# Kernel tuning notes

Hardware: AMD Instinct MI355X
Metric: run time of the kernel (lower is better)

Reference implementation:

```python
import jax, jax.numpy as jnp
import numpy as np

H = 256
W = 256
RADIUS = 1.5
TAU = 1.0
EPS = 1e-8


def _ndc_grid(h, w):
    ys, xs = jnp.meshgrid(jnp.arange(h, dtype=jnp.float32), jnp.arange(w, dtype=jnp.float32), indexing='ij')
    xs = xs / (w - 1) * 2.0 - 1.0
    ys = ys / (h - 1) * 2.0 - 1.0
    return jnp.stack([xs.ravel(), ys.ravel()], 0)  # [2, N]


def _make_rt(key, b, v):
    # near-identity extrinsics: identity rotation + small random translation
    t = jax.random.normal(key, (b, v, 3), dtype=jnp.float32) * 0.05
    rt = jnp.tile(jnp.eye(4, dtype=jnp.float32), (b, v, 1, 1))
    rt = rt.at[:, :, :3, 3].set(t)
    return rt


def setup_inputs() -> dict:
    key = jax.random.key(0)
    ks = jax.random.split(key, 4)
    B, V, C = 2, 3, 32
    depths = jax.random.uniform(ks[0], (B, V, 1, H, W), jnp.float32, 1.0, 3.0)
    feats = jax.random.normal(ks[1], (B, V, C, H, W), jnp.float32)
    K = jnp.tile(jnp.eye(4, dtype=jnp.float32), (B, 1, 1))
    K = K.at[:, 0, 0].set(1.2).at[:, 1, 1].set(1.2)  # NDC-space focal lengths
    src_RTs = _make_rt(ks[2], B, V)
    src_RTinvs = jnp.linalg.inv(src_RTs)
    dst_RTs = _make_rt(ks[3], B, 1)
    dst_RTinvs = jnp.linalg.inv(dst_RTs)
    return {"depths": depths, "feats": feats, "K": K, "src_RTs": src_RTs,
            "src_RTinvs": src_RTinvs, "dst_RTs": dst_RTs, "dst_RTinvs": dst_RTinvs}


def _view_to_world(depth, K_inv, RTinv):
    # depth: [BV, 1, N] -> world homogeneous coords [BV, 4, N]
    grid = _ndc_grid(H, W)                                      # [2, N]
    xy = grid[None] * depth                                     # [BV, 2, N]
    pc = jnp.concatenate([xy, depth, jnp.ones_like(depth)], 1)  # [BV, 4, N]
    cam = jnp.einsum('bij,bjn->bin', K_inv, pc)
    return jnp.einsum('bij,bjn->bin', RTinv, cam)


def _world_to_view(wrld, K, RT):
    cam = jnp.einsum('bij,bjn->bin', RT, wrld)
    proj = jnp.einsum('bij,bjn->bin', K, cam)
    z = proj[:, 2:3]
    xy = proj[:, 0:2] / (z + EPS)
    xy = jnp.where(z <= 0.0, -10.0, xy)       # invalid points pushed off-screen
    return jnp.concatenate([xy, z], 1)        # [BV, 3, N]


def _splatter(pc, feats, radius):
    # pc: [BV, N, 3] (x_ndc, y_ndc, depth); feats: [BV, C, N]
    BV, N, _ = pc.shape
    C = feats.shape[1]
    x, y, z = pc[..., 0], pc[..., 1], pc[..., 2]
    px = (x + 1.0) * 0.5 * (W - 1)
    py = (y + 1.0) * 0.5 * (H - 1)
    offs = jnp.array([[dy, dx] for dy in (-1, 0, 1) for dx in (-1, 0, 1)], dtype=jnp.float32)
    ix = jnp.round(px)[..., None] + offs[:, 1]     # [BV, N, 9]
    iy = jnp.round(py)[..., None] + offs[:, 0]
    dist = jnp.sqrt((ix - px[..., None]) ** 2 + (iy - py[..., None]) ** 2 + EPS)
    w_r = jnp.maximum(0.0, 1.0 - dist / radius)    # radius-based falloff
    valid = (ix >= 0) & (ix < W) & (iy >= 0) & (iy < H) & (z[..., None] > 0)
    w_d = jnp.exp(-TAU * z)[..., None]             # depth-aware (soft z-buffer) weight
    w = w_r * w_d * valid.astype(w_r.dtype)        # [BV, N, 9]
    idx = iy.astype(jnp.int32).clip(0, H - 1) * W + ix.astype(jnp.int32).clip(0, W - 1)
    flat = (jnp.arange(BV, dtype=jnp.int32)[:, None, None] * (H * W) + idx).reshape(-1)
    w_sum = jax.ops.segment_sum(w.reshape(-1), flat, num_segments=BV * H * W)
    fw = (feats[:, :, :, None] * w[:, None, :, :]).transpose(0, 2, 3, 1).reshape(-1, C)
    f_sum = jax.ops.segment_sum(fw, flat, num_segments=BV * H * W)
    z_sum = jax.ops.segment_sum((z[..., None] * w).reshape(-1), flat, num_segments=BV * H * W)
    out_f = (f_sum / (w_sum[:, None] + EPS)).reshape(BV, H, W, C).transpose(0, 3, 1, 2)
    out_d = (z_sum / (w_sum + EPS)).reshape(BV, 1, H, W)
    return out_f, out_d


def reference(depths, feats, K, src_RTs, src_RTinvs, dst_RTs, dst_RTinvs):
    B, V, C = feats.shape[0], feats.shape[1], feats.shape[2]
    N = H * W
    d = depths.reshape(B * V, 1, N)
    f = feats.reshape(B * V, C, N)
    K_bv = jnp.repeat(K, V, axis=0)
    K_inv_bv = jnp.repeat(jnp.linalg.inv(K), V, axis=0)
    src_rtinv = src_RTinvs.reshape(B * V, 4, 4)
    dst_rt = jnp.repeat(dst_RTs[:, 0], V, axis=0)
    wrld = _view_to_world(d, K_inv_bv, src_rtinv)      # view -> world per source view
    sampler = _world_to_view(wrld, K_bv, dst_rt)       # world -> target view [BV,3,N]
    pc = sampler.transpose(0, 2, 1)                    # [BV, N, 3]
    prj_f, prj_d = _splatter(pc, f, RADIUS)
    return prj_f.reshape(B, V, C, H, W), prj_d.reshape(B, V, 1, H, W)
```

## Files before the change

kernel.cpp:

```cpp
#include <hip/hip_runtime.h>
#include <hip/hip_fp16.h>
#include <math.h>

#define H 256
#define W 256
#define HW (H * W)
#define B 2
#define V 3
#define BV (B * V)
#define C 32
#define RADIUS 1.5f
#define TAU 1.0f
#define EPS 1e-8f

#define NPIX (BV * HW)
#define NBLK (NPIX / 256)

#define GW 258
#define GH 258
#define NCELL (BV * GH * GW)
#define NSUMS ((NCELL + 255) / 256)
#define ECAP 384

__device__ __forceinline__ int swizzle_block(int bid) {
    return (bid & 7) * (NBLK / 8) + (bid >> 3);
}

__global__ void setup_kernel(const float* __restrict__ Kmat,
                             const float* __restrict__ srcRTinv,
                             const float* __restrict__ dstRT,
                             float* __restrict__ Mbuf) {
    int bv = threadIdx.x;
    if (bv >= BV) return;
    int b = bv / V;

    float a[4][8];
    for (int i = 0; i < 4; i++)
        for (int j = 0; j < 4; j++) {
            a[i][j] = Kmat[b * 16 + i * 4 + j];
            a[i][4 + j] = (i == j) ? 1.0f : 0.0f;
        }
    for (int col = 0; col < 4; col++) {
        int piv = col;
        float best = fabsf(a[col][col]);
        for (int r = col + 1; r < 4; r++) {
            float v = fabsf(a[r][col]);
            if (v > best) { best = v; piv = r; }
        }
        if (piv != col) {
            for (int j = 0; j < 8; j++) {
                float t = a[col][j]; a[col][j] = a[piv][j]; a[piv][j] = t;
            }
        }
        float s = 1.0f / a[col][col];
        for (int j = 0; j < 8; j++) a[col][j] *= s;
        for (int r = 0; r < 4; r++) {
            if (r == col) continue;
            float m = a[r][col];
            for (int j = 0; j < 8; j++) a[r][j] -= m * a[col][j];
        }
    }
    float Kinv[16];
    for (int i = 0; i < 4; i++)
        for (int j = 0; j < 4; j++) Kinv[i * 4 + j] = a[i][4 + j];

    float T1[16];
    const float* S = srcRTinv + bv * 16;
    for (int i = 0; i < 4; i++)
        for (int j = 0; j < 4; j++) {
            float acc = 0.0f;
            for (int k = 0; k < 4; k++) acc += S[i * 4 + k] * Kinv[k * 4 + j];
            T1[i * 4 + j] = acc;
        }
    float T2[16];
    const float* D = dstRT + b * 16;
    for (int i = 0; i < 4; i++)
        for (int j = 0; j < 4; j++) {
            float acc = 0.0f;
            for (int k = 0; k < 4; k++) acc += D[i * 4 + k] * T1[k * 4 + j];
            T2[i * 4 + j] = acc;
        }
    const float* Kb = Kmat + b * 16;
    for (int i = 0; i < 4; i++)
        for (int j = 0; j < 4; j++) {
            float acc = 0.0f;
            for (int k = 0; k < 4; k++) acc += Kb[i * 4 + k] * T2[k * 4 + j];
            Mbuf[bv * 16 + i * 4 + j] = acc;
        }
}

__global__ __launch_bounds__(256) void project_count_kernel(
    const float* __restrict__ depths, const float* __restrict__ Mbuf,
    float4* __restrict__ staging, int2* __restrict__ meta) {
    int gid = swizzle_block(blockIdx.x) * 256 + threadIdx.x;
    int bv = gid >> 16;
    int n = gid & (HW - 1);

    float xn = (float)(n & (W - 1)) * (2.0f / (W - 1)) - 1.0f;
    float yn = (float)(n >> 8)      * (2.0f / (H - 1)) - 1.0f;
    float d = depths[gid];
    const float* M = Mbuf + bv * 16;
    float X = xn * d, Y = yn * d;
    float p0 = M[0] * X + M[1] * Y + M[2] * d + M[3];
    float p1 = M[4] * X + M[5] * Y + M[6] * d + M[7];
    float z  = M[8] * X + M[9] * Y + M[10] * d + M[11];

    int cell = -1;
    float px = 0.0f, py = 0.0f;
    if (z > 0.0f) {
        float inv = 1.0f / (z + EPS);
        px = (p0 * inv + 1.0f) * 0.5f * (float)(W - 1);
        py = (p1 * inv + 1.0f) * 0.5f * (float)(H - 1);
        float rx = rintf(px), ry = rintf(py);
        if (rx >= -1.0f && rx <= (float)W && ry >= -1.0f && ry <= (float)H) {
            cell = bv * (GH * GW) + ((int)ry + 1) * GW + ((int)rx + 1);
            atomicAdd(&meta[cell].y, 1);
        }
    }
    staging[gid] = make_float4(px, py, z, __int_as_float(cell));
}

__global__ __launch_bounds__(256) void alloc1_kernel(int2* __restrict__ meta,
                                                     int* __restrict__ bsum) {
    int i = blockIdx.x * 256 + threadIdx.x;
    int c = (i < NCELL) ? meta[i].y : 0;
    int lane = threadIdx.x & 63;
    int wid = threadIdx.x >> 6;
    int x = c;
#pragma unroll
    for (int dlt = 1; dlt < 64; dlt <<= 1) {
        int y = __shfl_up(x, dlt);
        if (lane >= dlt) x += y;
    }
    __shared__ int wsum[4];
    __shared__ int wbase[4];
    if (lane == 63) wsum[wid] = x;
    __syncthreads();
    if (threadIdx.x == 0) {
        int s0 = wsum[0], s1 = wsum[1], s2 = wsum[2], s3 = wsum[3];
        wbase[0] = 0; wbase[1] = s0; wbase[2] = s0 + s1; wbase[3] = s0 + s1 + s2;
        bsum[blockIdx.x] = s0 + s1 + s2 + s3;
    }
    __syncthreads();
    if (i <= NCELL) meta[i].x = wbase[wid] + (x - c);
}

__global__ __launch_bounds__(256) void alloc2_kernel(int* __restrict__ bsum) {
    __shared__ int wsum[4];
    __shared__ int wbase[4];
    __shared__ int carry_s;
    int tid = threadIdx.x;
    int lane = tid & 63;
    int wid = tid >> 6;
    if (tid == 0) carry_s = 0;
    __syncthreads();
    const int nchunk = (NSUMS + 255) / 256;
    for (int ch = 0; ch < nchunk; ch++) {
        int i = ch * 256 + tid;
        int c = (i < NSUMS) ? bsum[i] : 0;
        int x = c;
#pragma unroll
        for (int dlt = 1; dlt < 64; dlt <<= 1) {
            int y = __shfl_up(x, dlt);
            if (lane >= dlt) x += y;
        }
        if (lane == 63) wsum[wid] = x;
        __syncthreads();
        if (tid == 0) {
            int cr = carry_s;
            int s0 = wsum[0], s1 = wsum[1], s2 = wsum[2], s3 = wsum[3];
            wbase[0] = cr; wbase[1] = cr + s0; wbase[2] = cr + s0 + s1;
            wbase[3] = cr + s0 + s1 + s2;
            carry_s = cr + s0 + s1 + s2 + s3;
        }
        __syncthreads();
        if (i < NSUMS) bsum[i] = wbase[wid] + (x - c);
        __syncthreads();
    }
}

__global__ __launch_bounds__(256) void fill_kernel(
    const float* __restrict__ feats, const float4* __restrict__ staging,
    const int* __restrict__ bsum, int2* __restrict__ meta,
    float4* __restrict__ entries16, uint4* __restrict__ entriesF) {
    __shared__ float sm[C][257];
    int blk = blockIdx.x;
    int bv = blk >> 8;
    int n0 = (blk & 255) << 8;
    int tid = threadIdx.x;
    const float* src = feats + (size_t)bv * C * HW + n0;
#pragma unroll
    for (int c = 0; c < C; c++) sm[c][tid] = src[(size_t)c * HW + tid];
    __syncthreads();

    int gid = (bv << 16) | (n0 + tid);
    float4 s = staging[gid];
    int cell = __float_as_int(s.w);
    if (cell < 0) return;
    int pos = bsum[cell >> 8] + atomicAdd(&meta[cell].x, 1);

    float wd = expf(-TAU * s.z);
    entries16[pos] = make_float4(s.x, s.y, s.z, wd);

    uint4* dst = entriesF + (size_t)pos * 4;
#pragma unroll
    for (int g = 0; g < 4; g++) {
        __half2 h0 = __floats2half2_rn(sm[g * 8 + 0][tid], sm[g * 8 + 1][tid]);
        __half2 h1 = __floats2half2_rn(sm[g * 8 + 2][tid], sm[g * 8 + 3][tid]);
        __half2 h2 = __floats2half2_rn(sm[g * 8 + 4][tid], sm[g * 8 + 5][tid]);
        __half2 h3 = __floats2half2_rn(sm[g * 8 + 6][tid], sm[g * 8 + 7][tid]);
        uint4 pk;
        pk.x = *(unsigned int*)&h0;
        pk.y = *(unsigned int*)&h1;
        pk.z = *(unsigned int*)&h2;
        pk.w = *(unsigned int*)&h3;
        dst[g] = pk;
    }
}

__global__ __launch_bounds__(256) void gather_kernel(
    const float4* __restrict__ entries16, const uint4* __restrict__ entriesF,
    const int2* __restrict__ meta, const int* __restrict__ bsum,
    float* __restrict__ out) {
    __shared__ int cs_s[18][19];
    __shared__ int row_rs[18];
    __shared__ int row_off[18];
    __shared__ int row_sl[18];
    __shared__ float4 lds_e[ECAP];
    __shared__ uint4 lds_f[ECAP * 5];

    int sblk = swizzle_block(blockIdx.x);
    int bv = sblk >> 8;
    int t = sblk & 255;
    int ty0 = (t >> 4) << 4;
    int tx0 = (t & 15) << 4;
    int tid = threadIdx.x;
    int cellbase = bv * (GH * GW);

    for (int i = tid; i < 18 * 19; i += 256) {
        int hr = i / 19, lc = i - hr * 19;
        int cg = cellbase + (ty0 + hr) * GW + (tx0 + lc);
        int2 m = meta[cg];
        cs_s[hr][lc] = bsum[cg >> 8] + m.x - m.y;
    }
    __syncthreads();
    if (tid == 0) {
        int off = 0;
        for (int hr = 0; hr < 18; hr++) {
            int rs = cs_s[hr][0];
            int len = cs_s[hr][18] - rs;
            int sl = min(len, ECAP - off);
            if (sl < 0) sl = 0;
            row_rs[hr] = rs;
            row_off[hr] = off;
            row_sl[hr] = sl;
            off += sl;
        }
    }
    __syncthreads();
    {
        int wid = tid >> 6, lane = tid & 63;
        for (int hr = wid; hr < 18; hr += 4) {
            int rs = row_rs[hr], off = row_off[hr], sl = row_sl[hr];
            for (int j = lane; j < sl; j += 64)
                lds_e[off + j] = entries16[rs + j];
            int j0 = lane >> 2, g = lane & 3;
            for (int j = j0; j < sl; j += 16)
                lds_f[(off + j) * 5 + g] = entriesF[(size_t)(rs + j) * 4 + g];
        }
    }
    __syncthreads();

    int lx = tid & 15, ly = tid >> 4;
    float qx = (float)(tx0 + lx);
    float qy = (float)(ty0 + ly);

    float wsum = 0.0f, zwsum = 0.0f;
    float facc[C];
#pragma unroll
    for (int c = 0; c < C; c++) facc[c] = 0.0f;

    auto body = [&](int li) {
        float4 v = lds_e[li];
        uint4 fv0 = lds_f[li * 5 + 0];
        uint4 fv1 = lds_f[li * 5 + 1];
        uint4 fv2 = lds_f[li * 5 + 2];
        uint4 fv3 = lds_f[li * 5 + 3];
        float ddx = qx - v.x, ddy = qy - v.y;
        float dist = sqrtf(ddx * ddx + ddy * ddy + EPS);
        float wr = fmaxf(0.0f, 1.0f - dist * (1.0f / RADIUS));
        float w = wr * v.w;
        wsum += w;
        zwsum += v.z * w;
        const uint4* fvs[4] = {&fv0, &fv1, &fv2, &fv3};
#pragma unroll
        for (int g = 0; g < 4; g++) {
            const __half2* h2 = (const __half2*)fvs[g];
#pragma unroll
            for (int k = 0; k < 4; k++) {
                float2 f2 = __half22float2(h2[k]);
                facc[g * 8 + 2 * k]     = fmaf(w, f2.x, facc[g * 8 + 2 * k]);
                facc[g * 8 + 2 * k + 1] = fmaf(w, f2.y, facc[g * 8 + 2 * k + 1]);
            }
        }
    };
    auto accum_glb = [&](int pos) {
        float4 v = entries16[pos];
        float ddx = qx - v.x, ddy = qy - v.y;
        float d2 = ddx * ddx + ddy * ddy + EPS;
        if (d2 < RADIUS * RADIUS) {
            float dist = sqrtf(d2);
            float wr = 1.0f - dist * (1.0f / RADIUS);
            float w = wr * v.w;
            wsum += w;
            zwsum += v.z * w;
            const uint4* fp = entriesF + (size_t)pos * 4;
#pragma unroll
            for (int g = 0; g < 4; g++) {
                uint4 fv = fp[g];
                const __half2* h2 = (const __half2*)&fv;
#pragma unroll
                for (int k = 0; k < 4; k++) {
                    float2 f2 = __half22float2(h2[k]);
                    facc[g * 8 + 2 * k]     = fmaf(w, f2.x, facc[g * 8 + 2 * k]);
                    facc[g * 8 + 2 * k + 1] = fmaf(w, f2.y, facc[g * 8 + 2 * k + 1]);
                }
            }
        }
    };

#pragma unroll
    for (int dy = 0; dy < 3; dy++) {
        int hr = ly + dy;
        int s = cs_s[hr][lx];
        int e = cs_s[hr][lx + 3];
        int rs = row_rs[hr];
        int off = row_off[hr];
        int sEnd = rs + row_sl[hr];
        int e1 = min(e, sEnd);
        int li0 = off + (s - rs);
        int cnt = e1 - s;
        int j = 0;
        for (; j + 2 <= cnt; j += 2) {
            body(li0 + j);
            body(li0 + j + 1);
        }
        if (j < cnt) body(li0 + j);
        for (int pos = max(s, sEnd); pos < e; ++pos) accum_glb(pos);
    }

    int q = ((ty0 + ly) << 8) | (tx0 + lx);
    int gid = (bv << 16) | q;
    float invw = 1.0f / (wsum + EPS);
    float* ob = out + (size_t)bv * C * HW + q;
#pragma unroll
    for (int c = 0; c < C; c++) ob[(size_t)c * HW] = facc[c] * invw;
    out[(size_t)BV * C * HW + gid] = zwsum * invw;
}

extern "C" void kernel_launch(void* const* d_in, const int* in_sizes, int n_in,
                              void* d_out, int out_size, void* d_ws, size_t ws_size,
                              hipStream_t stream) {
    const float* depths   = (const float*)d_in[0];
    const float* feats    = (const float*)d_in[1];
    const float* Kmat     = (const float*)d_in[2];
    const float* srcRTinv = (const float*)d_in[4];
    const float* dstRT    = (const float*)d_in[5];
    float* out = (float*)d_out;

    char* ws = (char*)d_ws;
    size_t off_entriesF = 0;
    size_t off_entries16 = off_entriesF + (size_t)NPIX * 64;
    size_t off_staging = off_entries16 + (size_t)NPIX * 16;
    size_t off_meta = off_staging + (size_t)NPIX * 16;
    size_t off_bsum = off_meta + (size_t)(NCELL + 1) * 8;
    size_t off_M = off_bsum + (size_t)NSUMS * 4 + 16;
    size_t needed = off_M + (size_t)BV * 16 * 4;

    if (ws_size < needed) {
        hipMemsetAsync(d_out, 0, (size_t)out_size * 4, stream);
        return;
    }

    uint4* entriesF   = (uint4*)(ws + off_entriesF);
    float4* entries16 = (float4*)(ws + off_entries16);
    float4* staging   = (float4*)(ws + off_staging);
    int2* meta        = (int2*)(ws + off_meta);
    int* bsum         = (int*)(ws + off_bsum);
    float* Mbuf       = (float*)(ws + off_M);

    hipMemsetAsync(meta, 0, (size_t)(NCELL + 1) * 8, stream);
    setup_kernel<<<1, 64, 0, stream>>>(Kmat, srcRTinv, dstRT, Mbuf);
    project_count_kernel<<<NBLK, 256, 0, stream>>>(depths, Mbuf, staging, meta);
    alloc1_kernel<<<NSUMS, 256, 0, stream>>>(meta, bsum);
    alloc2_kernel<<<1, 256, 0, stream>>>(bsum);
    fill_kernel<<<NBLK, 256, 0, stream>>>(feats, staging, bsum, meta,
                                          entries16, entriesF);
    gather_kernel<<<NBLK, 256, 0, stream>>>(entries16, entriesF, meta, bsum,
                                            out);
}
```

Measured before the change: 181.5 us.

## Fold setup and second scan pass into neighbouring kernels, parallelize row offsets

Measured after the change: 291.8 us. +60.8%, slower.

```diff
diff --git a/kernel.cpp b/kernel.cpp
--- a/kernel.cpp
+++ b/kernel.cpp
@@ -26,14 +26,11 @@
     return (bid & 7) * (NBLK / 8) + (bid >> 3);
 }
 
-__global__ void setup_kernel(const float* __restrict__ Kmat,
-                             const float* __restrict__ srcRTinv,
-                             const float* __restrict__ dstRT,
-                             float* __restrict__ Mbuf) {
-    int bv = threadIdx.x;
-    if (bv >= BV) return;
+__device__ void compute_M(int bv, const float* __restrict__ Kmat,
+                          const float* __restrict__ srcRTinv,
+                          const float* __restrict__ dstRT,
+                          float* __restrict__ Mout) {
     int b = bv / V;
-
     float a[4][8];
     for (int i = 0; i < 4; i++)
         for (int j = 0; j < 4; j++) {
@@ -85,25 +82,28 @@
         for (int j = 0; j < 4; j++) {
             float acc = 0.0f;
             for (int k = 0; k < 4; k++) acc += Kb[i * 4 + k] * T2[k * 4 + j];
-            Mbuf[bv * 16 + i * 4 + j] = acc;
+            Mout[i * 4 + j] = acc;
         }
 }
 
 __global__ __launch_bounds__(256) void project_count_kernel(
-    const float* __restrict__ depths, const float* __restrict__ Mbuf,
+    const float* __restrict__ depths, const float* __restrict__ Kmat,
+    const float* __restrict__ srcRTinv, const float* __restrict__ dstRT,
     float4* __restrict__ staging, int2* __restrict__ meta) {
+    __shared__ float Msh[16];
     int gid = swizzle_block(blockIdx.x) * 256 + threadIdx.x;
     int bv = gid >> 16;
     int n = gid & (HW - 1);
+    if (threadIdx.x == 0) compute_M(bv, Kmat, srcRTinv, dstRT, Msh);
+    __syncthreads();
 
     float xn = (float)(n & (W - 1)) * (2.0f / (W - 1)) - 1.0f;
     float yn = (float)(n >> 8)      * (2.0f / (H - 1)) - 1.0f;
     float d = depths[gid];
-    const float* M = Mbuf + bv * 16;
     float X = xn * d, Y = yn * d;
-    float p0 = M[0] * X + M[1] * Y + M[2] * d + M[3];
-    float p1 = M[4] * X + M[5] * Y + M[6] * d + M[7];
-    float z  = M[8] * X + M[9] * Y + M[10] * d + M[11];
+    float p0 = Msh[0] * X + Msh[1] * Y + Msh[2]  * d + Msh[3];
+    float p1 = Msh[4] * X + Msh[5] * Y + Msh[6]  * d + Msh[7];
+    float z  = Msh[8] * X + Msh[9] * Y + Msh[10] * d + Msh[11];
 
     int cell = -1;
     float px = 0.0f, py = 0.0f;
@@ -120,8 +120,9 @@
     staging[gid] = make_float4(px, py, z, __int_as_float(cell));
 }
 
-__global__ __launch_bounds__(256) void alloc1_kernel(int2* __restrict__ meta,
-                                                     int* __restrict__ bsum) {
+__global__ __launch_bounds__(256) void alloc_kernel(int2* __restrict__ meta,
+                                                    int* __restrict__ bsum,
+                                                    int* __restrict__ done) {
     int i = blockIdx.x * 256 + threadIdx.x;
     int c = (i < NCELL) ? meta[i].y : 0;
     int lane = threadIdx.x & 63;
@@ -143,28 +144,29 @@
     }
     __syncthreads();
     if (i <= NCELL) meta[i].x = wbase[wid] + (x - c);
-}
-
-__global__ __launch_bounds__(256) void alloc2_kernel(int* __restrict__ bsum) {
-    __shared__ int wsum[4];
-    __shared__ int wbase[4];
+
+    __shared__ int ticket_s;
+    __threadfence();
+    if (threadIdx.x == 0) ticket_s = atomicAdd(done, 1);
+    __syncthreads();
+    if (ticket_s != NSUMS - 1) return;
+    __threadfence();
+
     __shared__ int carry_s;
     int tid = threadIdx.x;
-    int lane = tid & 63;
-    int wid = tid >> 6;
     if (tid == 0) carry_s = 0;
     __syncthreads();
     const int nchunk = (NSUMS + 255) / 256;
     for (int ch = 0; ch < nchunk; ch++) {
-        int i = ch * 256 + tid;
-        int c = (i < NSUMS) ? bsum[i] : 0;
-        int x = c;
+        int ii = ch * 256 + tid;
+        int cc = (ii < NSUMS) ? bsum[ii] : 0;
+        int xx = cc;
 #pragma unroll
         for (int dlt = 1; dlt < 64; dlt <<= 1) {
-            int y = __shfl_up(x, dlt);
-            if (lane >= dlt) x += y;
-        }
-        if (lane == 63) wsum[wid] = x;
+            int y = __shfl_up(xx, dlt);
+            if (lane >= dlt) xx += y;
+        }
+        if (lane == 63) wsum[wid] = xx;
         __syncthreads();
         if (tid == 0) {
             int cr = carry_s;
@@ -174,7 +176,7 @@
             carry_s = cr + s0 + s1 + s2 + s3;
         }
         __syncthreads();
-        if (i < NSUMS) bsum[i] = wbase[wid] + (x - c);
+        if (ii < NSUMS) bsum[ii] = wbase[wid] + (xx - cc);
         __syncthreads();
     }
 }
@@ -244,17 +246,24 @@
         cs_s[hr][lc] = bsum[cg >> 8] + m.x - m.y;
     }
     __syncthreads();
-    if (tid == 0) {
-        int off = 0;
-        for (int hr = 0; hr < 18; hr++) {
-            int rs = cs_s[hr][0];
-            int len = cs_s[hr][18] - rs;
-            int sl = min(len, ECAP - off);
+    if (tid < 32) {
+        int l = tid;
+        int start = 0, len = 0;
+        if (l < 18) { start = cs_s[l][0]; len = cs_s[l][18] - start; }
+        int x = len;
+#pragma unroll
+        for (int dlt = 1; dlt < 32; dlt <<= 1) {
+            int y = __shfl_up(x, dlt);
+            if (l >= dlt) x += y;
+        }
+        if (l < 18) {
+            int off = x - len;
+            row_rs[l] = start;
+            row_off[l] = off;
+            int sl = ECAP - off;
+            sl = min(sl, len);
             if (sl < 0) sl = 0;
-            row_rs[hr] = rs;
-            row_off[hr] = off;
-            row_sl[hr] = sl;
-            off += sl;
+            row_sl[l] = sl;
         }
     }
     __syncthreads();
@@ -373,9 +382,9 @@
     size_t off_entries16 = off_entriesF + (size_t)NPIX * 64;
     size_t off_staging = off_entries16 + (size_t)NPIX * 16;
     size_t off_meta = off_staging + (size_t)NPIX * 16;
-    size_t off_bsum = off_meta + (size_t)(NCELL + 1) * 8;
-    size_t off_M = off_bsum + (size_t)NSUMS * 4 + 16;
-    size_t needed = off_M + (size_t)BV * 16 * 4;
+    size_t off_done = off_meta + (size_t)(NCELL + 1) * 8;
+    size_t off_bsum = off_done + 16;
+    size_t needed = off_bsum + (size_t)NSUMS * 4 + 16;
 
     if (ws_size < needed) {
         hipMemsetAsync(d_out, 0, (size_t)out_size * 4, stream);
@@ -386,14 +395,13 @@
     float4* entries16 = (float4*)(ws + off_entries16);
     float4* staging   = (float4*)(ws + off_staging);
     int2* meta        = (int2*)(ws + off_meta);
+    int* done         = (int*)(ws + off_done);
     int* bsum         = (int*)(ws + off_bsum);
-    float* Mbuf       = (float*)(ws + off_M);
-
-    hipMemsetAsync(meta, 0, (size_t)(NCELL + 1) * 8, stream);
-    setup_kernel<<<1, 64, 0, stream>>>(Kmat, srcRTinv, dstRT, Mbuf);
-    project_count_kernel<<<NBLK, 256, 0, stream>>>(depths, Mbuf, staging, meta);
-    alloc1_kernel<<<NSUMS, 256, 0, stream>>>(meta, bsum);
-    alloc2_kernel<<<1, 256, 0, stream>>>(bsum);
+
+    hipMemsetAsync(meta, 0, (size_t)(NCELL + 1) * 8 + 16, stream);
+    project_count_kernel<<<NBLK, 256, 0, stream>>>(depths, Kmat, srcRTinv,
+                                                   dstRT, staging, meta);
+    alloc_kernel<<<NSUMS, 256, 0, stream>>>(meta, bsum, done);
     fill_kernel<<<NBLK, 256, 0, stream>>>(feats, staging, bsum, meta,
                                           entries16, entriesF);
     gather_kernel<<<NBLK, 256, 0, stream>>>(entries16, entriesF, meta, bsum,
```
